# Kernel optimization log

Measured on AMD Instinct MI355X. Metric: run time of the kernel, lower is better.

The kernel has to match this reference:

```python
import jax, jax.numpy as jnp
import numpy as np

DIM = 1024
HEADS = 16
DIM_HEAD = 64
INNER = HEADS * DIM_HEAD
EPS = 1e-5


def layernorm(x, g, b):
    mu = jnp.mean(x, axis=-1, keepdims=True)
    var = jnp.mean((x - mu) ** 2, axis=-1, keepdims=True)
    return (x - mu) * jax.lax.rsqrt(var + EPS) * g + b


def setup_inputs() -> dict:
    key = jax.random.key(0)
    ks = jax.random.split(key, 8)
    B, S = 2, 2048
    s_in = (2.0 / DIM) ** 0.5
    return {
        "x": jax.random.normal(ks[0], (B, S, DIM), jnp.float32),
        "w_qkv": jax.random.normal(ks[1], (DIM, 3 * INNER), jnp.float32) * s_in,
        "w_out": jax.random.normal(ks[2], (INNER, DIM), jnp.float32) * s_in,
        "b_out": jnp.zeros((DIM,), jnp.float32),
        "g1": jnp.ones((DIM,), jnp.float32),
        "beta1": jnp.zeros((DIM,), jnp.float32),
        "g2": jnp.ones((DIM,), jnp.float32),
        "beta2": jnp.zeros((DIM,), jnp.float32),
        "w_ff1": jax.random.normal(ks[3], (DIM, 4 * DIM), jnp.float32) * s_in,
        "b_ff1": jnp.zeros((4 * DIM,), jnp.float32),
        "w_ff2": jax.random.normal(ks[4], (4 * DIM, DIM), jnp.float32) * (2.0 / (4 * DIM)) ** 0.5,
        "b_ff2": jnp.zeros((DIM,), jnp.float32),
    }


def reference(x, w_qkv, w_out, b_out, g1, beta1, g2, beta2, w_ff1, b_ff1, w_ff2, b_ff2):
    B, S, D = x.shape
    scale = DIM_HEAD ** -0.5
    # --- attention block (pre-norm) ---
    h = layernorm(x, g1, beta1)
    qkv = h @ w_qkv  # [B,S,3*INNER]
    q, k, v = jnp.split(qkv, 3, axis=-1)
    def heads(t):
        return t.reshape(B, S, HEADS, DIM_HEAD).transpose(0, 2, 1, 3)  # [B,H,S,dh]
    q, k, v = heads(q), heads(k), heads(v)
    attn = jnp.einsum("bhsd,bhtd->bhst", q, k) * scale
    attn = jax.nn.softmax(attn, axis=-1)
    out = jnp.einsum("bhst,bhtd->bhsd", attn, v)
    out = out.transpose(0, 2, 1, 3).reshape(B, S, INNER)
    x = x + out @ w_out + b_out
    # --- FFN block (pre-norm) ---
    h = layernorm(x, g2, beta2)
    h = jax.nn.gelu(h @ w_ff1 + b_ff1, approximate=False)
    x = x + h @ w_ff2 + b_ff2
    return x
```

## Files before the change

kernel.cpp:

```cpp
#include <hip/hip_runtime.h>
#include <math.h>

typedef unsigned short u16;
typedef __attribute__((ext_vector_type(4))) float f32x4;
typedef __attribute__((ext_vector_type(16))) float f32x16;
typedef __attribute__((ext_vector_type(4))) unsigned short u16x4;
typedef __attribute__((ext_vector_type(8))) __bf16 bf16x8;

static constexpr int SS   = 2048;
static constexpr int DD   = 1024;
static constexpr int HH   = 16;
static constexpr int DH   = 64;
static constexpr int NTOK = 4096;
static constexpr int NQKV = 3072;

#define DEV static __device__ __forceinline__
#define GLD_AS1(p) ((__attribute__((address_space(1))) void*)(void*)(p))
#define GLD_AS3(p) ((__attribute__((address_space(3))) void*)(p))

#define WAIT_BAR(N) asm volatile("s_waitcnt vmcnt(" #N ")\n\ts_barrier" ::: "memory")
#define BAR()       asm volatile("s_barrier" ::: "memory")

DEV u16 f2bf(float f) {
    union { float f; unsigned int i; } v; v.f = f;
    unsigned int r = v.i + 0x7fffu + ((v.i >> 16) & 1u);
    return (u16)(r >> 16);
}
DEV float bdec(u16 u) {
    union { unsigned int i; float f; } v; v.i = ((unsigned int)u) << 16; return v.f;
}

DEV f32x4 MFMA(bf16x8 a, bf16x8 b, f32x4 c) {
    return __builtin_amdgcn_mfma_f32_16x16x32_bf16(a, b, c, 0, 0, 0);
}
DEV f32x16 MFMA32(bf16x8 a, bf16x8 b, f32x16 c) {
    return __builtin_amdgcn_mfma_f32_32x32x16_bf16(a, b, c, 0, 0, 0);
}
DEV f32x16 zero16() {
    f32x16 z;
    #pragma unroll
    for (int i = 0; i < 16; i++) z[i] = 0.f;
    return z;
}

__global__ __launch_bounds__(256)
void k_transpose(const float* __restrict__ in, u16* __restrict__ out, int R, int C) {
    __shared__ float tile[32][33];
    int c0 = blockIdx.x * 32, r0 = blockIdx.y * 32;
    int tx = threadIdx.x, ty = threadIdx.y;
    #pragma unroll
    for (int i = 0; i < 32; i += 8)
        tile[ty + i][tx] = in[(size_t)(r0 + ty + i) * C + c0 + tx];
    __syncthreads();
    #pragma unroll
    for (int i = 0; i < 32; i += 8)
        out[(size_t)(c0 + ty + i) * R + r0 + tx] = f2bf(tile[tx][ty + i]);
}

__global__ __launch_bounds__(256)
void k_transpose_v(const u16* __restrict__ qkv, u16* __restrict__ vT) {
    __shared__ u16 tile[32][33];
    int bid = blockIdx.x;
    int st = bid & 63;
    int dt = (bid >> 6) & 1;
    int bh = bid >> 7;
    int b = bh >> 4, h = bh & 15;
    int s0 = st * 32, d0 = dt * 32;
    int tx = threadIdx.x & 31, ty = threadIdx.x >> 5;
    const u16* src = qkv + ((size_t)(b * SS + s0)) * NQKV + 2048 + h * DH + d0;
    #pragma unroll
    for (int i = 0; i < 32; i += 8)
        tile[ty + i][tx] = src[(size_t)(ty + i) * NQKV + tx];
    __syncthreads();
    u16* dst = vT + ((size_t)bh * DH + d0) * SS + s0;
    #pragma unroll
    for (int i = 0; i < 32; i += 8)
        dst[(size_t)(ty + i) * SS + tx] = tile[tx][ty + i];
}

__global__ __launch_bounds__(256)
void k_layernorm(const float* __restrict__ x, const float* __restrict__ g,
                 const float* __restrict__ b, u16* __restrict__ out) {
    int row = blockIdx.x, t = threadIdx.x;
    const float4* xp = reinterpret_cast<const float4*>(x + (size_t)row * DD);
    float4 v = xp[t];
    float s = v.x + v.y + v.z + v.w;
    float q = v.x * v.x + v.y * v.y + v.z * v.z + v.w * v.w;
    #pragma unroll
    for (int m = 1; m < 64; m <<= 1) { s += __shfl_xor(s, m); q += __shfl_xor(q, m); }
    __shared__ float ps[4], pq[4];
    int w = t >> 6, l = t & 63;
    if (l == 0) { ps[w] = s; pq[w] = q; }
    __syncthreads();
    s = ps[0] + ps[1] + ps[2] + ps[3];
    q = pq[0] + pq[1] + pq[2] + pq[3];
    float mu = s * (1.0f / DD);
    float var = q * (1.0f / DD) - mu * mu;
    float rstd = rsqrtf(var + 1e-5f);
    float4 gv = reinterpret_cast<const float4*>(g)[t];
    float4 bv = reinterpret_cast<const float4*>(b)[t];
    u16x4 o;
    o.x = f2bf((v.x - mu) * rstd * gv.x + bv.x);
    o.y = f2bf((v.y - mu) * rstd * gv.y + bv.y);
    o.z = f2bf((v.z - mu) * rstd * gv.z + bv.z);
    o.w = f2bf((v.w - mu) * rstd * gv.w + bv.w);
    reinterpret_cast<u16x4*>(out + (size_t)row * DD)[t] = o;
}

__global__ __launch_bounds__(256)
void k_redln(const float* __restrict__ x, const u16* __restrict__ P0,
             const u16* __restrict__ P1, const float* __restrict__ bias,
             const float* __restrict__ g, const float* __restrict__ be,
             float* __restrict__ X1, u16* __restrict__ LNout) {
    int row = blockIdx.x, t = threadIdx.x;
    size_t i = (size_t)row * 256 + t;
    float4 xv = reinterpret_cast<const float4*>(x)[i];
    u16x4 a = reinterpret_cast<const u16x4*>(P0)[i];
    u16x4 bb = reinterpret_cast<const u16x4*>(P1)[i];
    float4 bv = reinterpret_cast<const float4*>(bias)[t];
    float4 v;
    v.x = xv.x + bdec(a.x) + bdec(bb.x) + bv.x;
    v.y = xv.y + bdec(a.y) + bdec(bb.y) + bv.y;
    v.z = xv.z + bdec(a.z) + bdec(bb.z) + bv.z;
    v.w = xv.w + bdec(a.w) + bdec(bb.w) + bv.w;
    reinterpret_cast<float4*>(X1)[i] = v;
    float s = v.x + v.y + v.z + v.w;
    float q = v.x * v.x + v.y * v.y + v.z * v.z + v.w * v.w;
    #pragma unroll
    for (int m = 1; m < 64; m <<= 1) { s += __shfl_xor(s, m); q += __shfl_xor(q, m); }
    __shared__ float ps[4], pq[4];
    int w = t >> 6, l = t & 63;
    if (l == 0) { ps[w] = s; pq[w] = q; }
    __syncthreads();
    s = ps[0] + ps[1] + ps[2] + ps[3];
    q = pq[0] + pq[1] + pq[2] + pq[3];
    float mu = s * (1.0f / DD);
    float var = q * (1.0f / DD) - mu * mu;
    float rstd = rsqrtf(var + 1e-5f);
    float4 gv = reinterpret_cast<const float4*>(g)[t];
    float4 ev = reinterpret_cast<const float4*>(be)[t];
    u16x4 o;
    o.x = f2bf((v.x - mu) * rstd * gv.x + ev.x);
    o.y = f2bf((v.y - mu) * rstd * gv.y + ev.y);
    o.z = f2bf((v.z - mu) * rstd * gv.z + ev.z);
    o.w = f2bf((v.w - mu) * rstd * gv.w + ev.w);
    reinterpret_cast<u16x4*>(LNout + (size_t)row * DD)[t] = o;
}

template<int MODE>
__global__ __launch_bounds__(512, 2)
void k_gemm256(const u16* __restrict__ A, const u16* __restrict__ BT,
               u16* __restrict__ Cb, const float* __restrict__ bias,
               int M, int N, int K) {
    __shared__ __align__(128) char lds[2][65536];
    const int t = threadIdx.x;
    const int w = t >> 6, l = t & 63;
    const int lg = l >> 4, lr = l & 15;
    const int m0 = blockIdx.y * 256, n0 = blockIdx.x * 256;
    const int wr = w >> 2, wc = w & 3;

    const int csw = ((l & 7) ^ (l >> 3)) << 3;
    const int srow = l >> 3;
    const int swzc = (lr & 7) << 4;

    f32x4 acc[8][4];
    #pragma unroll
    for (int i = 0; i < 8; i++)
        #pragma unroll
        for (int j = 0; j < 4; j++)
            acc[i][j] = (f32x4){0.f, 0.f, 0.f, 0.f};

    auto STAGE = [&](int buf, int kt) {
        char* base = lds[buf];
        #pragma unroll
        for (int i = 0; i < 4; i++) {
            const int chunk = w * 4 + i;
            const int r = chunk * 8 + srow;
            __builtin_amdgcn_global_load_lds(GLD_AS1(A  + (size_t)(m0 + r) * K + kt + csw),
                                             GLD_AS3(base + chunk * 1024), 16, 0, 0);
            __builtin_amdgcn_global_load_lds(GLD_AS1(BT + (size_t)(n0 + r) * K + kt + csw),
                                             GLD_AS3(base + 32768 + chunk * 1024), 16, 0, 0);
        }
    };

    STAGE(0, 0);
    int buf = 0;
    for (int kt = 0; kt < K; kt += 64) {
        if (kt + 64 < K) { STAGE(buf ^ 1, kt + 64); WAIT_BAR(8); }
        else            { WAIT_BAR(0); }
        const char* Abase = lds[buf];
        const char* Bbase = Abase + 32768;

        bf16x8 Bf[4][2];
        #pragma unroll
        for (int ni = 0; ni < 4; ni++)
            #pragma unroll
            for (int ks = 0; ks < 2; ks++)
                Bf[ni][ks] = *reinterpret_cast<const bf16x8*>(
                    Bbase + (wc * 64 + ni * 16 + lr) * 128 + ((ks * 64 + lg * 16) ^ swzc));

        #pragma unroll
        for (int mh = 0; mh < 4; mh++) {
            bf16x8 Af[2][2];
            #pragma unroll
            for (int mi2 = 0; mi2 < 2; mi2++)
                #pragma unroll
                for (int ks = 0; ks < 2; ks++)
                    Af[mi2][ks] = *reinterpret_cast<const bf16x8*>(
                        Abase + (wr * 128 + (mh * 2 + mi2) * 16 + lr) * 128 + ((ks * 64 + lg * 16) ^ swzc));
            BAR();
            __builtin_amdgcn_s_setprio(1);
            #pragma unroll
            for (int mi2 = 0; mi2 < 2; mi2++)
                #pragma unroll
                for (int ni = 0; ni < 4; ni++)
                    #pragma unroll
                    for (int ks = 0; ks < 2; ks++)
                        acc[mh * 2 + mi2][ni] = MFMA(Af[mi2][ks], Bf[ni][ks], acc[mh * 2 + mi2][ni]);
            __builtin_amdgcn_s_setprio(0);
            BAR();
        }
        buf ^= 1;
    }

    #pragma unroll
    for (int mi = 0; mi < 8; mi++) {
        #pragma unroll
        for (int ni = 0; ni < 4; ni++) {
            int nn = n0 + wc * 64 + ni * 16 + lr;
            #pragma unroll
            for (int r = 0; r < 4; r++) {
                int mm = m0 + wr * 128 + mi * 16 + lg * 4 + r;
                float v = acc[mi][ni][r];
                if (MODE == 0) {
                    float sv = (nn < 1024) ? v * 0.18033688011112042f : v;
                    Cb[(size_t)mm * NQKV + nn] = f2bf(sv);
                } else {
                    float u = v + bias[nn];
                    float u3 = u * u * u;
                    float gl = u / (1.0f + exp2f(-2.3022077f * u - 0.10294276f * u3));
                    Cb[(size_t)mm * N + nn] = f2bf(gl);
                }
            }
        }
    }
}

__global__ __launch_bounds__(256)
void k_gemm_sk(const u16* __restrict__ A, const u16* __restrict__ BT,
               u16* __restrict__ P0, u16* __restrict__ P1, int M, int N, int K) {
    __shared__ __align__(128) char lds[2][32768];
    const int t = threadIdx.x;
    const int w = t >> 6, l = t & 63;
    const int lg = l >> 4, lr = l & 15;
    const int m0 = blockIdx.y * 128, n0 = blockIdx.x * 128;
    const int wr = w >> 1, wc = w & 1;

    const int kh = K >> 1;
    const int kbeg = blockIdx.z * kh;
    const int kend = kbeg + kh;

    const int csw = ((l & 7) ^ (l >> 3)) << 3;
    const int chunk0 = w * 4;
    const int srow = (l >> 3);

    f32x4 acc[4][4];
    #pragma unroll
    for (int i = 0; i < 4; i++)
        #pragma unroll
        for (int j = 0; j < 4; j++)
            acc[i][j] = (f32x4){0.f, 0.f, 0.f, 0.f};

    #pragma unroll
    for (int i = 0; i < 4; i++) {
        const int chunk = chunk0 + i;
        const int r = chunk * 8 + srow;
        __builtin_amdgcn_global_load_lds(GLD_AS1(A  + (size_t)(m0 + r) * K + kbeg + csw),
                                         GLD_AS3(lds[0] + chunk * 1024), 16, 0, 0);
        __builtin_amdgcn_global_load_lds(GLD_AS1(BT + (size_t)(n0 + r) * K + kbeg + csw),
                                         GLD_AS3(lds[0] + 16384 + chunk * 1024), 16, 0, 0);
    }

    int buf = 0;
    for (int kt = kbeg; kt < kend; kt += 64) {
        if (kt + 64 < kend) {
            #pragma unroll
            for (int i = 0; i < 4; i++) {
                const int chunk = chunk0 + i;
                const int r = chunk * 8 + srow;
                __builtin_amdgcn_global_load_lds(GLD_AS1(A  + (size_t)(m0 + r) * K + kt + 64 + csw),
                                                 GLD_AS3(lds[buf ^ 1] + chunk * 1024), 16, 0, 0);
                __builtin_amdgcn_global_load_lds(GLD_AS1(BT + (size_t)(n0 + r) * K + kt + 64 + csw),
                                                 GLD_AS3(lds[buf ^ 1] + 16384 + chunk * 1024), 16, 0, 0);
            }
            WAIT_BAR(8);
        } else {
            WAIT_BAR(0);
        }
        const char* Al = lds[buf];
        const char* Bl = lds[buf] + 16384;
        #pragma unroll
        for (int s = 0; s < 2; s++) {
            const int swz = (s * 64 + lg * 16) ^ ((lr & 7) << 4);
            bf16x8 af[4], bfr[4];
            #pragma unroll
            for (int mi = 0; mi < 4; mi++)
                af[mi] = *reinterpret_cast<const bf16x8*>(Al + (wr * 64 + mi * 16 + lr) * 128 + swz);
            #pragma unroll
            for (int ni = 0; ni < 4; ni++)
                bfr[ni] = *reinterpret_cast<const bf16x8*>(Bl + (wc * 64 + ni * 16 + lr) * 128 + swz);
            #pragma unroll
            for (int mi = 0; mi < 4; mi++)
                #pragma unroll
                for (int ni = 0; ni < 4; ni++)
                    acc[mi][ni] = MFMA(af[mi], bfr[ni], acc[mi][ni]);
        }
        BAR();
        buf ^= 1;
    }

    u16* dst = blockIdx.z ? P1 : P0;
    #pragma unroll
    for (int mi = 0; mi < 4; mi++) {
        #pragma unroll
        for (int ni = 0; ni < 4; ni++) {
            int nn = n0 + wc * 64 + ni * 16 + lr;
            #pragma unroll
            for (int r = 0; r < 4; r++) {
                int mm = m0 + wr * 64 + mi * 16 + lg * 4 + r;
                dst[(size_t)mm * N + nn] = f2bf(acc[mi][ni][r]);
            }
        }
    }
}

__global__ __launch_bounds__(256)
void k_ffreduce(const float* __restrict__ RES, const u16* __restrict__ P0,
                const u16* __restrict__ P1, const float* __restrict__ bias,
                float* __restrict__ OUT) {
    int i = blockIdx.x * 256 + threadIdx.x;
    float4 xv = reinterpret_cast<const float4*>(RES)[i];
    u16x4 a = reinterpret_cast<const u16x4*>(P0)[i];
    u16x4 b = reinterpret_cast<const u16x4*>(P1)[i];
    float4 bv = reinterpret_cast<const float4*>(bias)[i & (DD / 4 - 1)];
    float4 o;
    o.x = xv.x + bdec(a.x) + bdec(b.x) + bv.x;
    o.y = xv.y + bdec(a.y) + bdec(b.y) + bv.y;
    o.z = xv.z + bdec(a.z) + bdec(b.z) + bv.z;
    o.w = xv.w + bdec(a.w) + bdec(b.w) + bv.w;
    reinterpret_cast<float4*>(OUT)[i] = o;
}

__global__ __launch_bounds__(256)
void k_attn(const u16* __restrict__ qkv, const u16* __restrict__ vT,
            u16* __restrict__ out) {
    const int w = threadIdx.x >> 6, l = threadIdx.x & 63;
    const int q = l & 31, hi = l >> 5;
    const int task = (blockIdx.x & 7) * 64 + (blockIdx.x >> 3);
    const int bh = task >> 4;
    const int qg = task & 15;
    const int b = bh >> 4, h = bh & 15;
    const size_t rowbase = (size_t)b * SS;
    const int q0 = (qg * 4 + w) * 32;

    __shared__ __align__(128) u16 Kl[3][64 * 64];
    __shared__ __align__(128) u16 Vl[2][64 * 64];

    const u16* kbase = qkv + rowbase * NQKV + 1024 + h * DH;
    const u16* vbase = vT + (size_t)bh * DH * SS;

    const int srow8 = l >> 3;
    const int sslot = (l & 7) ^ srow8;
    const int kr0 = w * 8 + srow8;
    const u16* kg0 = kbase + (size_t)kr0 * NQKV + sslot * 8;
    const u16* kg1 = kbase + (size_t)(kr0 + 32) * NQKV + sslot * 8;
    const u16* vg0 = vbase + (size_t)kr0 * SS + sslot * 8;
    const u16* vg1 = vbase + (size_t)(kr0 + 32) * SS + sslot * 8;
    const int chA = (w * 8) * 64, chB = (w * 8 + 32) * 64;

    const u16* qrow = qkv + (rowbase + q0 + q) * NQKV + h * DH + hi * 8;
    bf16x8 qf[4];
    #pragma unroll
    for (int ks = 0; ks < 4; ks++)
        qf[ks] = *reinterpret_cast<const bf16x8*>(qrow + ks * 16);
    asm volatile("s_waitcnt vmcnt(0)" ::: "memory");

    bf16x8 onesf;
    #pragma unroll
    for (int i = 0; i < 8; i++) onesf[i] = (__bf16)1.0f;

    f32x16 o0 = zero16(), o1 = zero16();
    f32x16 lacc = zero16();
    const int qsw = (q & 7) << 3;

    __builtin_amdgcn_global_load_lds(GLD_AS1(kg0), GLD_AS3((u16*)Kl[0] + chA), 16, 0, 0);
    __builtin_amdgcn_global_load_lds(GLD_AS1(kg1), GLD_AS3((u16*)Kl[0] + chB), 16, 0, 0);
    __builtin_amdgcn_global_load_lds(GLD_AS1(kg0 + (size_t)64 * NQKV), GLD_AS3((u16*)Kl[1] + chA), 16, 0, 0);
    __builtin_amdgcn_global_load_lds(GLD_AS1(kg1 + (size_t)64 * NQKV), GLD_AS3((u16*)Kl[1] + chB), 16, 0, 0);
    __builtin_amdgcn_global_load_lds(GLD_AS1(vg0), GLD_AS3((u16*)Vl[0] + chA), 16, 0, 0);
    __builtin_amdgcn_global_load_lds(GLD_AS1(vg1), GLD_AS3((u16*)Vl[0] + chB), 16, 0, 0);
    WAIT_BAR(4);

    f32x16 scA0 = zero16(), scA1 = zero16();
    {
        const u16* Kb = Kl[0];
        #pragma unroll
        for (int ks = 0; ks < 4; ks++) {
            const int off = (ks * 16 + hi * 8) ^ qsw;
            bf16x8 kf0 = *reinterpret_cast<const bf16x8*>(Kb + q * 64 + off);
            bf16x8 kf1 = *reinterpret_cast<const bf16x8*>(Kb + (q + 32) * 64 + off);
            scA0 = MFMA32(kf0, qf[ks], scA0);
            scA1 = MFMA32(kf1, qf[ks], scA1);
        }
    }

    int kRead = 1, vRead = 0;
    for (int i = 0; i < 32; ++i) {
        const int kStage = (kRead == 2) ? 0 : kRead + 1;
        if (i + 2 < 32) {
            const size_t koff = (size_t)(i + 2) * 64 * NQKV;
            __builtin_amdgcn_global_load_lds(GLD_AS1(kg0 + koff), GLD_AS3((u16*)Kl[kStage] + chA), 16, 0, 0);
            __builtin_amdgcn_global_load_lds(GLD_AS1(kg1 + koff), GLD_AS3((u16*)Kl[kStage] + chB), 16, 0, 0);
            WAIT_BAR(2);
        } else {
            WAIT_BAR(0);
        }
        if (i + 1 < 32) {
            const int voff = (i + 1) * 64;
            __builtin_amdgcn_global_load_lds(GLD_AS1(vg0 + voff), GLD_AS3((u16*)Vl[vRead ^ 1] + chA), 16, 0, 0);
            __builtin_amdgcn_global_load_lds(GLD_AS1(vg1 + voff), GLD_AS3((u16*)Vl[vRead ^ 1] + chB), 16, 0, 0);
        }

        f32x16 p0, p1;
        #pragma unroll
        for (int j = 0; j < 16; j++) p0[j] = exp2f(scA0[j]);
        #pragma unroll
        for (int j = 0; j < 16; j++) p1[j] = exp2f(scA1[j]);

        f32x16 stB0 = zero16(), stB1 = zero16();
        if (i + 1 < 32) {
            const u16* Kb = Kl[kRead];
            #pragma unroll
            for (int ks = 0; ks < 4; ks++) {
                const int off = (ks * 16 + hi * 8) ^ qsw;
                bf16x8 kf0 = *reinterpret_cast<const bf16x8*>(Kb + q * 64 + off);
                bf16x8 kf1 = *reinterpret_cast<const bf16x8*>(Kb + (q + 32) * 64 + off);
                stB0 = MFMA32(kf0, qf[ks], stB0);
                stB1 = MFMA32(kf1, qf[ks], stB1);
            }
        }

        union W { unsigned int u; __bf16 h[2]; };
        W pw[16];
        #pragma unroll
        for (int m = 0; m < 8; m++) {
            pw[m].h[0] = (__bf16)p0[2 * m];
            pw[m].h[1] = (__bf16)p0[2 * m + 1];
            pw[8 + m].h[0] = (__bf16)p1[2 * m];
            pw[8 + m].h[1] = (__bf16)p1[2 * m + 1];
        }
        bf16x8 pf[4];
        #pragma unroll
        for (int kk = 0; kk < 4; kk++) {
            const int base = (kk >> 1) * 8 + (kk & 1) * 4;
            unsigned int a0 = pw[base + 0].u, a1 = pw[base + 1].u;
            unsigned int b0 = pw[base + 2].u, b1 = pw[base + 3].u;
            unsigned int own0 = hi ? b0 : a0, own1 = hi ? b1 : a1;
            unsigned int snd0 = hi ? a0 : b0, snd1 = hi ? a1 : b1;
            unsigned int r0 = __shfl_xor(snd0, 32), r1 = __shfl_xor(snd1, 32);
            union F { unsigned int u[4]; bf16x8 v; } f;
            f.u[0] = hi ? r0 : own0;
            f.u[1] = hi ? r1 : own1;
            f.u[2] = hi ? own0 : r0;
            f.u[3] = hi ? own1 : r1;
            pf[kk] = f.v;
        }

        const u16* Vb = Vl[vRead];
        #pragma unroll
        for (int kk = 0; kk < 4; kk++) {
            const int off = (kk * 16 + hi * 8) ^ qsw;
            bf16x8 v0 = *reinterpret_cast<const bf16x8*>(Vb + q * 64 + off);
            bf16x8 v1 = *reinterpret_cast<const bf16x8*>(Vb + (q + 32) * 64 + off);
            lacc = MFMA32(onesf, pf[kk], lacc);
            o0 = MFMA32(v0, pf[kk], o0);
            o1 = MFMA32(v1, pf[kk], o1);
        }

        scA0 = stB0;
        scA1 = stB1;
        kRead = kStage;
        vRead ^= 1;
    }

    float invl = 1.0f / lacc[0];
    u16* orow = out + (rowbase + q0 + q) * DD + h * DH + hi * 4;
    #pragma unroll
    for (int a = 0; a < 4; a++) {
        u16x4 s0v, s1v;
        #pragma unroll
        for (int i = 0; i < 4; i++) {
            s0v[i] = f2bf(o0[4 * a + i] * invl);
            s1v[i] = f2bf(o1[4 * a + i] * invl);
        }
        *reinterpret_cast<u16x4*>(orow + 8 * a)      = s0v;
        *reinterpret_cast<u16x4*>(orow + 32 + 8 * a) = s1v;
    }
}

extern "C" void kernel_launch(void* const* d_in, const int* in_sizes, int n_in,
                              void* d_out, int out_size, void* d_ws, size_t ws_size,
                              hipStream_t stream) {
    (void)in_sizes; (void)n_in; (void)out_size; (void)ws_size;
    const float* x     = (const float*)d_in[0];
    const float* w_qkv = (const float*)d_in[1];
    const float* w_out = (const float*)d_in[2];
    const float* b_out = (const float*)d_in[3];
    const float* g1    = (const float*)d_in[4];
    const float* be1   = (const float*)d_in[5];
    const float* g2    = (const float*)d_in[6];
    const float* be2   = (const float*)d_in[7];
    const float* w_ff1 = (const float*)d_in[8];
    const float* b_ff1 = (const float*)d_in[9];
    const float* w_ff2 = (const float*)d_in[10];
    const float* b_ff2 = (const float*)d_in[11];

    char* ws = (char*)d_ws;
    u16*   W  = (u16*)(ws);
    u16*   Hb = (u16*)(ws + 8388608);
    u16*   QF = (u16*)(ws + 16777216);
    u16*   VT = (u16*)(ws + 50331648);
    u16*   AO = (u16*)(ws + 58720256);
    float* X1 = (float*)(ws + 67108864);
    float* OUT = (float*)d_out;

    k_layernorm<<<NTOK, 256, 0, stream>>>(x, g1, be1, Hb);
    k_transpose<<<dim3(3072 / 32, 1024 / 32), dim3(32, 8), 0, stream>>>(w_qkv, W, 1024, 3072);
    k_gemm256<0><<<dim3(3072 / 256, 4096 / 256), 512, 0, stream>>>(
        Hb, W, QF, nullptr, NTOK, NQKV, 1024);
    k_transpose_v<<<4096, 256, 0, stream>>>(QF, VT);
    k_attn<<<512, 256, 0, stream>>>(QF, VT, AO);
    k_transpose<<<dim3(1024 / 32, 1024 / 32), dim3(32, 8), 0, stream>>>(w_out, W, 1024, 1024);
    k_gemm_sk<<<dim3(1024 / 128, 4096 / 128, 2), 256, 0, stream>>>(
        AO, W, Hb, VT, NTOK, 1024, 1024);
    k_redln<<<NTOK, 256, 0, stream>>>(x, Hb, VT, b_out, g2, be2, X1, AO);
    k_transpose<<<dim3(4096 / 32, 1024 / 32), dim3(32, 8), 0, stream>>>(w_ff1, W, 1024, 4096);
    k_gemm256<2><<<dim3(4096 / 256, 4096 / 256), 512, 0, stream>>>(
        AO, W, QF, b_ff1, NTOK, 4096, 1024);
    k_transpose<<<dim3(1024 / 32, 4096 / 32), dim3(32, 8), 0, stream>>>(w_ff2, W, 4096, 1024);
    k_gemm_sk<<<dim3(1024 / 128, 4096 / 128, 2), 256, 0, stream>>>(
        QF, W, VT, Hb, NTOK, 1024, 4096);
    k_ffreduce<<<NTOK * DD / 4 / 256, 256, 0, stream>>>(X1, VT, Hb, b_ff2, OUT);
}
```

Measured before the change: 262.2 us.

## Use 128x128 tiles for QKV GEMM and interleave staging in FF1 GEMM

The QKV projection moves from the 256x256 templated GEMM (192 blocks) to a dedicated 128x128-tile kernel with 256 threads (768 blocks), so the grid fills the GPU's compute units better. The FF1 GEMM now splits its next-tile global-to-LDS staging into four quarter loads, issued between the compute phases, and waits only for the first part before reading B fragments. It also drops the extra barrier before each MFMA group. The smaller QKV tiles give less data reuse per block, and the reworked FF1 pipeline changes LDS row placement and the synchronisation points.

```diff
diff --git a/kernel.cpp b/kernel.cpp
--- a/kernel.cpp
+++ b/kernel.cpp
@@ -147,11 +147,95 @@
     reinterpret_cast<u16x4*>(LNout + (size_t)row * DD)[t] = o;
 }
 
-template<int MODE>
+__global__ __launch_bounds__(256)
+void k_gemm_qkv(const u16* __restrict__ A, const u16* __restrict__ BT,
+                u16* __restrict__ Cb, int M, int N, int K) {
+    __shared__ __align__(128) char lds[2][32768];
+    const int t = threadIdx.x;
+    const int w = t >> 6, l = t & 63;
+    const int lg = l >> 4, lr = l & 15;
+    const int m0 = blockIdx.y * 128, n0 = blockIdx.x * 128;
+    const int wr = w >> 1, wc = w & 1;
+
+    const int csw = ((l & 7) ^ (l >> 3)) << 3;
+    const int chunk0 = w * 4;
+    const int srow = (l >> 3);
+
+    f32x4 acc[4][4];
+    #pragma unroll
+    for (int i = 0; i < 4; i++)
+        #pragma unroll
+        for (int j = 0; j < 4; j++)
+            acc[i][j] = (f32x4){0.f, 0.f, 0.f, 0.f};
+
+    #pragma unroll
+    for (int i = 0; i < 4; i++) {
+        const int chunk = chunk0 + i;
+        const int r = chunk * 8 + srow;
+        __builtin_amdgcn_global_load_lds(GLD_AS1(A  + (size_t)(m0 + r) * K + csw),
+                                         GLD_AS3(lds[0] + chunk * 1024), 16, 0, 0);
+        __builtin_amdgcn_global_load_lds(GLD_AS1(BT + (size_t)(n0 + r) * K + csw),
+                                         GLD_AS3(lds[0] + 16384 + chunk * 1024), 16, 0, 0);
+    }
+
+    int buf = 0;
+    for (int kt = 0; kt < K; kt += 64) {
+        if (kt + 64 < K) {
+            #pragma unroll
+            for (int i = 0; i < 4; i++) {
+                const int chunk = chunk0 + i;
+                const int r = chunk * 8 + srow;
+                __builtin_amdgcn_global_load_lds(GLD_AS1(A  + (size_t)(m0 + r) * K + kt + 64 + csw),
+                                                 GLD_AS3(lds[buf ^ 1] + chunk * 1024), 16, 0, 0);
+                __builtin_amdgcn_global_load_lds(GLD_AS1(BT + (size_t)(n0 + r) * K + kt + 64 + csw),
+                                                 GLD_AS3(lds[buf ^ 1] + 16384 + chunk * 1024), 16, 0, 0);
+            }
+            WAIT_BAR(8);
+        } else {
+            WAIT_BAR(0);
+        }
+        const char* Al = lds[buf];
+        const char* Bl = lds[buf] + 16384;
+        #pragma unroll
+        for (int s = 0; s < 2; s++) {
+            const int swz = (s * 64 + lg * 16) ^ ((lr & 7) << 4);
+            bf16x8 af[4], bfr[4];
+            #pragma unroll
+            for (int mi = 0; mi < 4; mi++)
+                af[mi] = *reinterpret_cast<const bf16x8*>(Al + (wr * 64 + mi * 16 + lr) * 128 + swz);
+            #pragma unroll
+            for (int ni = 0; ni < 4; ni++)
+                bfr[ni] = *reinterpret_cast<const bf16x8*>(Bl + (wc * 64 + ni * 16 + lr) * 128 + swz);
+            #pragma unroll
+            for (int mi = 0; mi < 4; mi++)
+                #pragma unroll
+                for (int ni = 0; ni < 4; ni++)
+                    acc[mi][ni] = MFMA(af[mi], bfr[ni], acc[mi][ni]);
+        }
+        BAR();
+        buf ^= 1;
+    }
+
+    #pragma unroll
+    for (int mi = 0; mi < 4; mi++) {
+        #pragma unroll
+        for (int ni = 0; ni < 4; ni++) {
+            int nn = n0 + wc * 64 + ni * 16 + lr;
+            #pragma unroll
+            for (int r = 0; r < 4; r++) {
+                int mm = m0 + wr * 64 + mi * 16 + lg * 4 + r;
+                float v = acc[mi][ni][r];
+                float sv = (nn < 1024) ? v * 0.18033688011112042f : v;
+                Cb[(size_t)mm * NQKV + nn] = f2bf(sv);
+            }
+        }
+    }
+}
+
 __global__ __launch_bounds__(512, 2)
-void k_gemm256(const u16* __restrict__ A, const u16* __restrict__ BT,
-               u16* __restrict__ Cb, const float* __restrict__ bias,
-               int M, int N, int K) {
+void k_gemm_ff1(const u16* __restrict__ A, const u16* __restrict__ BT,
+                u16* __restrict__ Cb, const float* __restrict__ bias,
+                int M, int N, int K) {
     __shared__ __align__(128) char lds[2][65536];
     const int t = threadIdx.x;
     const int w = t >> 6, l = t & 63;
@@ -160,7 +244,7 @@
     const int wr = w >> 2, wc = w & 3;
 
     const int csw = ((l & 7) ^ (l >> 3)) << 3;
-    const int srow = l >> 3;
+    const int srow8 = l >> 3;
     const int swzc = (lr & 7) << 4;
 
     f32x4 acc[8][4];
@@ -170,45 +254,50 @@
         for (int j = 0; j < 4; j++)
             acc[i][j] = (f32x4){0.f, 0.f, 0.f, 0.f};
 
-    auto STAGE = [&](int buf, int kt) {
-        char* base = lds[buf];
-        #pragma unroll
-        for (int i = 0; i < 4; i++) {
-            const int chunk = w * 4 + i;
-            const int r = chunk * 8 + srow;
-            __builtin_amdgcn_global_load_lds(GLD_AS1(A  + (size_t)(m0 + r) * K + kt + csw),
-                                             GLD_AS3(base + chunk * 1024), 16, 0, 0);
-            __builtin_amdgcn_global_load_lds(GLD_AS1(BT + (size_t)(n0 + r) * K + kt + csw),
-                                             GLD_AS3(base + 32768 + chunk * 1024), 16, 0, 0);
+    auto STAGEH = [&](int bf, int which, int half, int kt) {
+        const u16* sb = which ? BT : A;
+        const int rb = which ? n0 : m0;
+        char* dst = lds[bf] + which * 32768 + half * 16384 + w * 1024;
+        #pragma unroll
+        for (int j = 0; j < 2; j++) {
+            const int r = half * 128 + (j * 8 + w) * 8 + srow8;
+            __builtin_amdgcn_global_load_lds(GLD_AS1(sb + (size_t)(rb + r) * K + kt + csw),
+                                             GLD_AS3(dst + j * 8192), 16, 0, 0);
         }
     };
 
-    STAGE(0, 0);
+    STAGEH(0, 0, 0, 0); STAGEH(0, 0, 1, 0); STAGEH(0, 1, 0, 0); STAGEH(0, 1, 1, 0);
+
+    const int nt = K >> 6;
     int buf = 0;
-    for (int kt = 0; kt < K; kt += 64) {
-        if (kt + 64 < K) { STAGE(buf ^ 1, kt + 64); WAIT_BAR(8); }
-        else            { WAIT_BAR(0); }
+    for (int tt = 0; tt < nt; ++tt) {
+        const int nb = buf ^ 1;
+        const bool pre = (tt + 1 < nt);
         const char* Abase = lds[buf];
-        const char* Bbase = Abase + 32768;
+        const char* Bbase = lds[buf] + 32768;
 
         bf16x8 Bf[4][2];
         #pragma unroll
-        for (int ni = 0; ni < 4; ni++)
-            #pragma unroll
-            for (int ks = 0; ks < 2; ks++)
-                Bf[ni][ks] = *reinterpret_cast<const bf16x8*>(
-                    Bbase + (wc * 64 + ni * 16 + lr) * 128 + ((ks * 64 + lg * 16) ^ swzc));
-
-        #pragma unroll
-        for (int mh = 0; mh < 4; mh++) {
+        for (int p = 0; p < 4; p++) {
+            if (pre) STAGEH(nb, p >> 1, p & 1, (tt + 1) * 64);
+            if (p == 0) {
+                if (pre) { WAIT_BAR(2); } else { WAIT_BAR(0); }
+                #pragma unroll
+                for (int ni = 0; ni < 4; ni++)
+                    #pragma unroll
+                    for (int ks = 0; ks < 2; ks++)
+                        Bf[ni][ks] = *reinterpret_cast<const bf16x8*>(
+                            Bbase + (wc >> 1) * 16384 + ((wc & 1) * 64 + ni * 16 + lr) * 128
+                                  + ((ks * 64 + lg * 16) ^ swzc));
+            }
             bf16x8 Af[2][2];
             #pragma unroll
             for (int mi2 = 0; mi2 < 2; mi2++)
                 #pragma unroll
                 for (int ks = 0; ks < 2; ks++)
                     Af[mi2][ks] = *reinterpret_cast<const bf16x8*>(
-                        Abase + (wr * 128 + (mh * 2 + mi2) * 16 + lr) * 128 + ((ks * 64 + lg * 16) ^ swzc));
-            BAR();
+                        Abase + wr * 16384 + ((p * 2 + mi2) * 16 + lr) * 128
+                              + ((ks * 64 + lg * 16) ^ swzc));
             __builtin_amdgcn_s_setprio(1);
             #pragma unroll
             for (int mi2 = 0; mi2 < 2; mi2++)
@@ -216,11 +305,11 @@
                 for (int ni = 0; ni < 4; ni++)
                     #pragma unroll
                     for (int ks = 0; ks < 2; ks++)
-                        acc[mh * 2 + mi2][ni] = MFMA(Af[mi2][ks], Bf[ni][ks], acc[mh * 2 + mi2][ni]);
+                        acc[p * 2 + mi2][ni] = MFMA(Af[mi2][ks], Bf[ni][ks], acc[p * 2 + mi2][ni]);
             __builtin_amdgcn_s_setprio(0);
             BAR();
         }
-        buf ^= 1;
+        buf = nb;
     }
 
     #pragma unroll
@@ -231,16 +320,10 @@
             #pragma unroll
             for (int r = 0; r < 4; r++) {
                 int mm = m0 + wr * 128 + mi * 16 + lg * 4 + r;
-                float v = acc[mi][ni][r];
-                if (MODE == 0) {
-                    float sv = (nn < 1024) ? v * 0.18033688011112042f : v;
-                    Cb[(size_t)mm * NQKV + nn] = f2bf(sv);
-                } else {
-                    float u = v + bias[nn];
-                    float u3 = u * u * u;
-                    float gl = u / (1.0f + exp2f(-2.3022077f * u - 0.10294276f * u3));
-                    Cb[(size_t)mm * N + nn] = f2bf(gl);
-                }
+                float u = acc[mi][ni][r] + bias[nn];
+                float u3 = u * u * u;
+                float gl = u / (1.0f + exp2f(-2.3022077f * u - 0.10294276f * u3));
+                Cb[(size_t)mm * N + nn] = f2bf(gl);
             }
         }
     }
@@ -536,8 +619,8 @@
 
     k_layernorm<<<NTOK, 256, 0, stream>>>(x, g1, be1, Hb);
     k_transpose<<<dim3(3072 / 32, 1024 / 32), dim3(32, 8), 0, stream>>>(w_qkv, W, 1024, 3072);
-    k_gemm256<0><<<dim3(3072 / 256, 4096 / 256), 512, 0, stream>>>(
-        Hb, W, QF, nullptr, NTOK, NQKV, 1024);
+    k_gemm_qkv<<<dim3(3072 / 128, 4096 / 128), 256, 0, stream>>>(
+        Hb, W, QF, NTOK, NQKV, 1024);
     k_transpose_v<<<4096, 256, 0, stream>>>(QF, VT);
     k_attn<<<512, 256, 0, stream>>>(QF, VT, AO);
     k_transpose<<<dim3(1024 / 32, 1024 / 32), dim3(32, 8), 0, stream>>>(w_out, W, 1024, 1024);
@@ -545,7 +628,7 @@
         AO, W, Hb, VT, NTOK, 1024, 1024);
     k_redln<<<NTOK, 256, 0, stream>>>(x, Hb, VT, b_out, g2, be2, X1, AO);
     k_transpose<<<dim3(4096 / 32, 1024 / 32), dim3(32, 8), 0, stream>>>(w_ff1, W, 1024, 4096);
-    k_gemm256<2><<<dim3(4096 / 256, 4096 / 256), 512, 0, stream>>>(
+    k_gemm_ff1<<<dim3(4096 / 256, 4096 / 256), 512, 0, stream>>>(
         AO, W, QF, b_ff1, NTOK, 4096, 1024);
     k_transpose<<<dim3(1024 / 32, 4096 / 32), dim3(32, 8), 0, stream>>>(w_ff2, W, 4096, 1024);
     k_gemm_sk<<<dim3(1024 / 128, 4096 / 128, 2), 256, 0, stream>>>(
```

Result: faster. 253.4 us (-3.4%).
